# Kernel tuning notes

Measured on AMD Instinct MI355X. Metric: run time of the kernel, lower is better.

## Reference

```python
import jax, jax.numpy as jnp
import numpy as np

B, H, W, C = 2, 96, 96, 96
GROUPS = 32
EPS = 1e-5


def group_norm_dim1(x, gamma, beta):
    # Faithful to torch nn.GroupNorm(32, C) applied to an NHWC tensor:
    # dim 1 (H) is treated as the channel axis, normalized over (H//G, W, C) per group.
    b, h, w, c = x.shape
    xg = x.reshape(b, GROUPS, h // GROUPS, w, c)
    mean = xg.mean(axis=(2, 3, 4), keepdims=True)
    var = xg.var(axis=(2, 3, 4), keepdims=True)
    xn = ((xg - mean) * jax.lax.rsqrt(var + EPS)).reshape(b, h, w, c)
    return xn * gamma[None, :, None, None] + beta[None, :, None, None]


def setup_inputs() -> dict:
    key = jax.random.key(0)
    ks = jax.random.split(key, 9)
    s = 1.0 / np.sqrt(C)  # kaiming-uniform-ish scale
    x = jax.random.normal(ks[0], (B, H, W, C), dtype=jnp.float32)
    Wq = jax.random.uniform(ks[1], (C, C), jnp.float32, -s, s)
    Wk = jax.random.uniform(ks[2], (C, C), jnp.float32, -s, s)
    Wv = jax.random.uniform(ks[3], (C, C), jnp.float32, -s, s)
    Wp = jax.random.uniform(ks[4], (C, C), jnp.float32, -s, s)
    return {
        "x": x,
        "gamma": jnp.ones((H,), jnp.float32),   # GroupNorm affine weight (over dim 1)
        "beta": jnp.zeros((H,), jnp.float32),
        "Wq": Wq, "bq": jnp.zeros((C,), jnp.float32),
        "Wk": Wk, "bk": jnp.zeros((C,), jnp.float32),
        "Wv": Wv, "bv": jnp.zeros((C,), jnp.float32),
        "Wp": Wp, "bp": jnp.zeros((C,), jnp.float32),
    }


def reference(x, gamma, beta, Wq, bq, Wk, bk, Wv, bv, Wp, bp):
    b, h, w, c = x.shape
    hn = group_norm_dim1(x, gamma, beta)
    q = hn @ Wq + bq  # [B,H,W,C], Nin = contract last dim
    k = hn @ Wk + bk
    v = hn @ Wv + bv
    scale = c ** (-0.5)
    # full dense spatial attention: [B, HW, HW]
    scores = jnp.einsum('bxyc,buvc->bxyuv', q, k) * scale
    attn = jax.nn.softmax(scores.reshape(b, h, w, h * w), axis=-1).reshape(b, h, w, h, w)
    o = jnp.einsum('bxyuv,buvc->bxyc', attn, v)
    return x + (o @ Wp + bp)
```

## Files before the change

### kernel.cpp

```cpp
#include <hip/hip_runtime.h>
#include <hip/hip_bf16.h>
#include <stdint.h>

#define B_   2
#define H_   96
#define W_   96
#define C_   96
#define HW_  (H_ * W_)
#define NT_  (B_ * HW_)
#define EPS_ 1e-5f
#define SCL (0.10206207261596575f * 1.4426950408889634f)

typedef __hip_bfloat16 bf16;
typedef __attribute__((ext_vector_type(8))) short short8;
typedef __attribute__((ext_vector_type(16))) float f32x16;

__device__ __forceinline__ uint32_t pk_bf16(float a, float b) {
    uint32_t ua = __float_as_uint(a) + 0x8000u;
    uint32_t ub = __float_as_uint(b) + 0x8000u;
    return __builtin_amdgcn_perm(ub, ua, 0x07060302u);
}
__device__ __forceinline__ float bl(uint32_t u) { uint32_t x = u << 16;         return *(float*)&x; }
__device__ __forceinline__ float bh(uint32_t u) { uint32_t x = u & 0xffff0000u; return *(float*)&x; }
__device__ __forceinline__ float fexp2(float x) { return __builtin_amdgcn_exp2f(x); }
__device__ __forceinline__ short8 lds_frag(const short* p) {
    union { int2 h[2]; short8 v; } t;
    t.h[0] = *(const int2*)(p);
    t.h[1] = *(const int2*)(p + 4);
    return t.v;
}

__device__ __forceinline__ void load_hn_frags(
        const float* __restrict__ x, const float2* __restrict__ stats,
        const float* __restrict__ gamma, const float* __restrict__ beta,
        int token, int hh, short8* hf) {
    int b = token / HW_;
    int h = (token % HW_) / W_;
    float2 st = stats[b * 32 + h / 3];
    float g0 = gamma[h];
    float ga = g0 * st.y;
    float be = beta[h] - st.x * st.y * g0;
    const float* xr = x + (size_t)token * C_ + hh * 8;
    #pragma unroll
    for (int s = 0; s < 6; ++s) {
        float4 a = *(const float4*)(xr + s * 16);
        float4 c = *(const float4*)(xr + s * 16 + 4);
        union { uint32_t w[4]; short8 v; } f;
        f.w[0] = pk_bf16(a.x * ga + be, a.y * ga + be);
        f.w[1] = pk_bf16(a.z * ga + be, a.w * ga + be);
        f.w[2] = pk_bf16(c.x * ga + be, c.y * ga + be);
        f.w[3] = pk_bf16(c.z * ga + be, c.w * ga + be);
        hf[s] = f.v;
    }
}

__global__ __launch_bounds__(1024)
void stats_prep_kernel(const float* __restrict__ x, float2* __restrict__ stats,
                       const float* __restrict__ Wq, const float* __restrict__ Wk,
                       const float* __restrict__ Wv, const float* __restrict__ Wp,
                       bf16* __restrict__ wqt, bf16* __restrict__ wkt,
                       bf16* __restrict__ wvt, bf16* __restrict__ wpt) {
    int blk = blockIdx.x;
    int tid = threadIdx.x;
    if (blk >= 64) {
        int wsel = blk - 64;
        const float* S = (wsel == 0) ? Wq : (wsel == 1) ? Wk : (wsel == 2) ? Wv : Wp;
        bf16* D = (wsel == 0) ? wqt : (wsel == 1) ? wkt : (wsel == 2) ? wvt : wpt;
        for (int i = tid; i < C_ * C_; i += 1024) {
            int r = i / C_, c = i % C_;
            D[c * C_ + r] = __float2bfloat16(S[r * C_ + c]);
        }
        return;
    }
    int b = blk >> 5, g = blk & 31;
    const int n4 = 3 * W_ * C_ / 4;
    const float4* xb = (const float4*)(x + (size_t)(b * H_ + 3 * g) * (W_ * C_));
    float s = 0.f, ss = 0.f;
    for (int i = tid; i < n4; i += 1024) {
        float4 v = xb[i];
        s  += v.x + v.y + v.z + v.w;
        ss += v.x * v.x + v.y * v.y + v.z * v.z + v.w * v.w;
    }
    #pragma unroll
    for (int off = 1; off < 64; off <<= 1) {
        s  += __shfl_xor(s, off, 64);
        ss += __shfl_xor(ss, off, 64);
    }
    __shared__ float rs[16], rss[16];
    int wid = tid >> 6;
    if ((tid & 63) == 0) { rs[wid] = s; rss[wid] = ss; }
    __syncthreads();
    if (tid == 0) {
        float ts = 0.f, tss = 0.f;
        #pragma unroll
        for (int i = 0; i < 16; ++i) { ts += rs[i]; tss += rss[i]; }
        const float n = 3 * W_ * C_;
        float mean = ts / n;
        float var  = tss / n - mean * mean;
        stats[blk] = make_float2(mean, rsqrtf(var + EPS_));
    }
}

__global__ __launch_bounds__(64)
void qkv_kernel(const float* __restrict__ x, const float2* __restrict__ stats,
                const float* __restrict__ gamma, const float* __restrict__ beta,
                const bf16* __restrict__ wqt, const bf16* __restrict__ wkt,
                const bf16* __restrict__ wvt,
                const float* __restrict__ bq, const float* __restrict__ bk,
                const float* __restrict__ bv,
                bf16* __restrict__ qb, bf16* __restrict__ kb, bf16* __restrict__ vt) {
    __shared__ short tile_s[96 * 36];

    int blk = blockIdx.x;
    int w = blk / 576, tile = blk % 576;
    int n0 = tile * 32;
    int lane = threadIdx.x;
    int col = lane & 31, hh = lane >> 5;
    int token = n0 + col;

    short8 hf[6];
    load_hn_frags(x, stats, gamma, beta, token, hh, hf);

    if (w == 2) {
        int bb = n0 / HW_, nl0 = n0 % HW_;
        #pragma unroll
        for (int t = 0; t < 3; ++t) {
            int c = t * 32 + col;
            const bf16* wrow = wvt + (size_t)c * C_ + hh * 8;
            f32x16 acc = (f32x16)(0.f);
            #pragma unroll
            for (int s = 0; s < 6; ++s)
                acc = __builtin_amdgcn_mfma_f32_32x32x16_bf16(
                        hf[s], *(const short8*)(wrow + s * 16), acc, 0, 0, 0);
            float bias = bv[c];
            short* dst = tile_s + c * 36 + 4 * hh;
            #pragma unroll
            for (int g = 0; g < 4; ++g) {
                int2 pk = make_int2(pk_bf16(acc[4 * g] + bias, acc[4 * g + 1] + bias),
                                    pk_bf16(acc[4 * g + 2] + bias, acc[4 * g + 3] + bias));
                *(int2*)(dst + 8 * g) = pk;
            }
        }
        __syncthreads();
        bf16* vbase = vt + (size_t)bb * C_ * HW_ + nl0;
        #pragma unroll
        for (int i = 0; i < 6; ++i) {
            int pos = lane + 64 * i;
            int ch = pos >> 2, q4 = pos & 3;
            short8 vv = lds_frag(tile_s + ch * 36 + q4 * 8);
            *(short8*)(vbase + (size_t)ch * HW_ + q4 * 8) = vv;
        }
    } else {
        const bf16*  wt   = (w == 0) ? wqt : wkt;
        const float* bias = (w == 0) ? bq : bk;
        bf16*        dst  = (w == 0) ? qb : kb;
        float        scl  = (w == 0) ? SCL : 1.f;
        #pragma unroll
        for (int t = 0; t < 3; ++t) {
            const bf16* wrow = wt + (size_t)(t * 32 + col) * C_ + hh * 8;
            f32x16 acc = (f32x16)(0.f);
            #pragma unroll
            for (int s = 0; s < 6; ++s)
                acc = __builtin_amdgcn_mfma_f32_32x32x16_bf16(
                        *(const short8*)(wrow + s * 16), hf[s], acc, 0, 0, 0);
            #pragma unroll
            for (int g = 0; g < 4; ++g) {
                int nb = t * 32 + 8 * g + 4 * hh;
                float4 b4 = *(const float4*)(bias + nb);
                float v0 = (acc[4 * g]     + b4.x) * scl;
                float v1 = (acc[4 * g + 1] + b4.y) * scl;
                float v2 = (acc[4 * g + 2] + b4.z) * scl;
                float v3 = (acc[4 * g + 3] + b4.w) * scl;
                *(int2*)(tile_s + col * 100 + nb) =
                    make_int2(pk_bf16(v0, v1), pk_bf16(v2, v3));
            }
        }
        __syncthreads();
        bf16* dbase = dst + (size_t)n0 * C_;
        #pragma unroll
        for (int i = 0; i < 6; ++i) {
            int pos = lane + 64 * i;
            int tok = pos / 12, ch8 = (pos % 12) * 8;
            short8 vv = lds_frag(tile_s + tok * 100 + ch8);
            *(short8*)(dbase + tok * C_ + ch8) = vv;
        }
    }
}

template<int KS, int LOG2KS>
__global__ __launch_bounds__(256, 2)
void attn_kernel(const bf16* __restrict__ qb, const bf16* __restrict__ kb,
                 const bf16* __restrict__ vt,
                 bf16* __restrict__ pob, float* __restrict__ pl) {
    constexpr int KRANGE  = HW_ / KS;
    constexpr int ATT_NIT = KRANGE / 32;

    __shared__ short Kbuf[2][32 * 100];
    __shared__ short Vbuf[2][96 * 36];

    int blk = blockIdx.x;
    int ks = blk & (KS - 1), qg = blk >> LOG2KS;
    int b = qg / 36, g36 = qg % 36;
    int n0 = g36 * 256;
    int tid = threadIdx.x;
    int wave = tid >> 6, lane = tid & 63;
    int col = lane & 31, hh = lane >> 5;

    const bf16* kbb = kb + ((size_t)b * HW_ + (size_t)ks * KRANGE) * C_;
    const bf16* vbb = vt + (size_t)b * C_ * HW_ + (size_t)ks * KRANGE;

    int nA = n0 + wave * 32 + col;
    int nB = nA + 128;
    short8 qfA[6], qfB[6];
    {
        const bf16* qrowA = qb + (size_t)(b * HW_ + nA) * C_ + hh * 8;
        const bf16* qrowB = qb + (size_t)(b * HW_ + nB) * C_ + hh * 8;
        #pragma unroll
        for (int s = 0; s < 6; ++s) qfA[s] = *(const short8*)(qrowA + s * 16);
        #pragma unroll
        for (int s = 0; s < 6; ++s) qfB[s] = *(const short8*)(qrowB + s * 16);
    }

    f32x16 oaA[3], oaB[3];
    #pragma unroll
    for (int t = 0; t < 3; ++t) { oaA[t] = (f32x16)(0.f); oaB[t] = (f32x16)(0.f); }
    float lA = 0.f, lB = 0.f;

    bool isK = (tid < 128);
    int t128 = tid & 127;
    int ldsA[3], ldsB[3], goff[3];
    #pragma unroll
    for (int j = 0; j < 3; ++j) {
        int c = t128 + 128 * j;
        if (isK) {
            ldsA[j] = (c / 12) * 100 + (c % 12) * 8;
            ldsB[j] = ldsA[j] + 4;
            goff[j] = c * 8;
        } else {
            int rw = c >> 2, g = c & 3;
            ldsA[j] = rw * 36 + (2 * g - (g & 1)) * 4;
            ldsB[j] = rw * 36 + (2 * g + 2 - (g & 1)) * 4;
            goff[j] = rw * HW_ + g * 8;
        }
    }
    const bf16* gbase = isK ? kbb : vbb;
    const int itstep = isK ? (32 * C_) : 32;

    {
        short* sb = isK ? Kbuf[0] : Vbuf[0];
        #pragma unroll
        for (int j = 0; j < 3; ++j) {
            int4 r = *(const int4*)(gbase + goff[j]);
            *(int2*)(sb + ldsA[j]) = make_int2(r.x, r.y);
            *(int2*)(sb + ldsB[j]) = make_int2(r.z, r.w);
        }
    }
    __syncthreads();

    union FU { uint32_t w[4]; short8 v; };

    for (int it = 0; it < ATT_NIT; ++it) {
        int cur = it & 1;
        bool pre = (it + 1 < ATT_NIT);
        int4 r0, r1, r2;
        if (pre) {
            const bf16* g = gbase + (size_t)(it + 1) * itstep;
            r0 = *(const int4*)(g + goff[0]);
            r1 = *(const int4*)(g + goff[1]);
            r2 = *(const int4*)(g + goff[2]);
        }

        const short* Kc = Kbuf[cur];
        const short* Vc = Vbuf[cur];

        short8 kf[6];
        #pragma unroll
        for (int s = 0; s < 6; ++s)
            kf[s] = lds_frag(Kc + col * 100 + s * 16 + hh * 8);

        f32x16 stA = (f32x16)(0.f);
        #pragma unroll
        for (int s = 0; s < 6; ++s)
            stA = __builtin_amdgcn_mfma_f32_32x32x16_bf16(kf[s], qfA[s], stA, 0, 0, 0);
        f32x16 stB = (f32x16)(0.f);
        #pragma unroll
        for (int s = 0; s < 6; ++s)
            stB = __builtin_amdgcn_mfma_f32_32x32x16_bf16(kf[s], qfB[s], stB, 0, 0, 0);

        FU f0A, f1A, f0B, f1B;
        {
            float p[16], ls = 0.f;
            #pragma unroll
            for (int i = 0; i < 16; ++i) { p[i] = fexp2(stA[i]); ls += p[i]; }
            lA += ls;
            #pragma unroll
            for (int j = 0; j < 4; ++j) {
                f0A.w[j] = pk_bf16(p[2 * j],     p[2 * j + 1]);
                f1A.w[j] = pk_bf16(p[8 + 2 * j], p[8 + 2 * j + 1]);
            }
        }
        {
            float p[16], ls = 0.f;
            #pragma unroll
            for (int i = 0; i < 16; ++i) { p[i] = fexp2(stB[i]); ls += p[i]; }
            lB += ls;
            #pragma unroll
            for (int j = 0; j < 4; ++j) {
                f0B.w[j] = pk_bf16(p[2 * j],     p[2 * j + 1]);
                f1B.w[j] = pk_bf16(p[8 + 2 * j], p[8 + 2 * j + 1]);
            }
        }

        #pragma unroll
        for (int t = 0; t < 3; ++t) {
            const short* vr = Vc + (32 * t + col) * 36 + hh * 8;
            short8 vf0 = lds_frag(vr);
            short8 vf1 = lds_frag(vr + 16);
            oaA[t] = __builtin_amdgcn_mfma_f32_32x32x16_bf16(vf0, f0A.v, oaA[t], 0, 0, 0);
            oaA[t] = __builtin_amdgcn_mfma_f32_32x32x16_bf16(vf1, f1A.v, oaA[t], 0, 0, 0);
            oaB[t] = __builtin_amdgcn_mfma_f32_32x32x16_bf16(vf0, f0B.v, oaB[t], 0, 0, 0);
            oaB[t] = __builtin_amdgcn_mfma_f32_32x32x16_bf16(vf1, f1B.v, oaB[t], 0, 0, 0);
        }

        if (pre) {
            short* sb = isK ? Kbuf[cur ^ 1] : Vbuf[cur ^ 1];
            *(int2*)(sb + ldsA[0]) = make_int2(r0.x, r0.y);
            *(int2*)(sb + ldsB[0]) = make_int2(r0.z, r0.w);
            *(int2*)(sb + ldsA[1]) = make_int2(r1.x, r1.y);
            *(int2*)(sb + ldsB[1]) = make_int2(r1.z, r1.w);
            *(int2*)(sb + ldsA[2]) = make_int2(r2.x, r2.y);
            *(int2*)(sb + ldsB[2]) = make_int2(r2.z, r2.w);
        }
        __syncthreads();
    }

    {
        size_t bqA = (size_t)b * HW_ + nA;
        size_t bqB = (size_t)b * HW_ + nB;
        float ltA = lA + __shfl_xor(lA, 32, 64);
        float ltB = lB + __shfl_xor(lB, 32, 64);
        if (hh == 0) {
            pl[(size_t)ks * NT_ + bqA] = ltA;
            pl[(size_t)ks * NT_ + bqB] = ltB;
        }
        #pragma unroll
        for (int t = 0; t < 3; ++t)
            #pragma unroll
            for (int g = 0; g < 4; ++g) {
                int c0 = t * 32 + 8 * g + 4 * hh;
                uint2 pkA = make_uint2(
                    pk_bf16(oaA[t][4 * g],     oaA[t][4 * g + 1]),
                    pk_bf16(oaA[t][4 * g + 2], oaA[t][4 * g + 3]));
                *(uint2*)(pob + ((size_t)ks * NT_ + bqA) * C_ + c0) = pkA;
                uint2 pkB = make_uint2(
                    pk_bf16(oaB[t][4 * g],     oaB[t][4 * g + 1]),
                    pk_bf16(oaB[t][4 * g + 2], oaB[t][4 * g + 3]));
                *(uint2*)(pob + ((size_t)ks * NT_ + bqB) * C_ + c0) = pkB;
            }
    }
}

template<int KS>
__global__ __launch_bounds__(256)
void out_kernel(const float* __restrict__ x,
                const bf16* __restrict__ pob, const float* __restrict__ pl,
                const bf16* __restrict__ wpt, const float* __restrict__ bp,
                float* __restrict__ out) {
    __shared__ short ofs[32 * 100];
    __shared__ float linv_s[32];

    int tile = blockIdx.x;
    int n0 = tile * 32;
    int tid = threadIdx.x;

    if (tid < 32) {
        int token = n0 + tid;
        float l = 0.f;
        #pragma unroll
        for (int ksp = 0; ksp < KS; ++ksp) l += pl[(size_t)ksp * NT_ + token];
        linv_s[tid] = 1.f / l;
    }
    __syncthreads();

    for (int pos = tid; pos < 384; pos += 256) {
        int token = pos / 12, c8 = (pos % 12) * 8;
        float acc[8] = {0.f, 0.f, 0.f, 0.f, 0.f, 0.f, 0.f, 0.f};
        #pragma unroll
        for (int ksp = 0; ksp < KS; ++ksp) {
            uint4 u = *(const uint4*)(pob + ((size_t)ksp * NT_ + n0 + token) * C_ + c8);
            acc[0] += bl(u.x); acc[1] += bh(u.x);
            acc[2] += bl(u.y); acc[3] += bh(u.y);
            acc[4] += bl(u.z); acc[5] += bh(u.z);
            acc[6] += bl(u.w); acc[7] += bh(u.w);
        }
        float inv = linv_s[token];
        short* dst = ofs + token * 100 + c8;
        *(int2*)(dst)     = make_int2(pk_bf16(acc[0] * inv, acc[1] * inv),
                                      pk_bf16(acc[2] * inv, acc[3] * inv));
        *(int2*)(dst + 4) = make_int2(pk_bf16(acc[4] * inv, acc[5] * inv),
                                      pk_bf16(acc[6] * inv, acc[7] * inv));
    }
    __syncthreads();

    int wave = tid >> 6;
    if (wave >= 3) return;
    int lane = tid & 63, col = lane & 31, hh = lane >> 5;
    int t = wave;
    int token = n0 + col;

    short8 of[6];
    #pragma unroll
    for (int s = 0; s < 6; ++s)
        of[s] = lds_frag(ofs + col * 100 + s * 16 + hh * 8);

    f32x16 acc = (f32x16)(0.f);
    const bf16* wrow = wpt + (size_t)(t * 32 + col) * C_ + hh * 8;
    #pragma unroll
    for (int s = 0; s < 6; ++s)
        acc = __builtin_amdgcn_mfma_f32_32x32x16_bf16(
                *(const short8*)(wrow + s * 16), of[s], acc, 0, 0, 0);
    #pragma unroll
    for (int g = 0; g < 4; ++g) {
        int nb = t * 32 + 8 * g + 4 * hh;
        float4 b4 = *(const float4*)(bp + nb);
        float4 xv = *(const float4*)(x + (size_t)token * C_ + nb);
        float4 rr;
        rr.x = xv.x + acc[4 * g]     + b4.x;
        rr.y = xv.y + acc[4 * g + 1] + b4.y;
        rr.z = xv.z + acc[4 * g + 2] + b4.z;
        rr.w = xv.w + acc[4 * g + 3] + b4.w;
        *(float4*)(out + (size_t)token * C_ + nb) = rr;
    }
}

extern "C" void kernel_launch(void* const* d_in, const int* in_sizes, int n_in,
                              void* d_out, int out_size, void* d_ws, size_t ws_size,
                              hipStream_t stream) {
    const float* x     = (const float*)d_in[0];
    const float* gamma = (const float*)d_in[1];
    const float* beta  = (const float*)d_in[2];
    const float* Wq    = (const float*)d_in[3];
    const float* bq    = (const float*)d_in[4];
    const float* Wk    = (const float*)d_in[5];
    const float* bk    = (const float*)d_in[6];
    const float* Wv    = (const float*)d_in[7];
    const float* bv    = (const float*)d_in[8];
    const float* Wp    = (const float*)d_in[9];
    const float* bp    = (const float*)d_in[10];
    float* out = (float*)d_out;

    char* ws = (char*)d_ws;
    const size_t TB = (size_t)NT_ * C_ * 2;
    bf16* qb  = (bf16*)(ws);
    bf16* kb  = (bf16*)(ws + TB);
    bf16* vt  = (bf16*)(ws + 2 * TB);
    bf16* wqt = (bf16*)(ws + 3 * TB);
    bf16* wkt = (bf16*)(ws + 3 * TB + 18432);
    bf16* wvt = (bf16*)(ws + 3 * TB + 2 * 18432);
    bf16* wpt = (bf16*)(ws + 3 * TB + 3 * 18432);
    float2* stats = (float2*)(ws + 3 * TB + 4 * 18432);
    bf16*  pob = (bf16*)(ws + 3 * TB + 4 * 18432 + 512);

    hipLaunchKernelGGL(stats_prep_kernel, dim3(68), dim3(1024), 0, stream,
                       x, stats, Wq, Wk, Wv, Wp, wqt, wkt, wvt, wpt);
    hipLaunchKernelGGL(qkv_kernel, dim3(3 * 576), dim3(64), 0, stream,
                       x, stats, gamma, beta, wqt, wkt, wvt, bq, bk, bv, qb, kb, vt);

    const size_t base   = 3 * TB + 4 * 18432 + 512;
    const size_t need16 = base + (size_t)16 * NT_ * C_ * 2 + (size_t)16 * NT_ * 4;
    if (ws_size >= need16) {
        float* pl = (float*)(ws + base + (size_t)16 * NT_ * C_ * 2);
        hipLaunchKernelGGL((attn_kernel<16, 4>), dim3(16 * 72), dim3(256), 0, stream,
                           qb, kb, vt, pob, pl);
        hipLaunchKernelGGL((out_kernel<16>), dim3(576), dim3(256), 0, stream,
                           x, pob, pl, wpt, bp, out);
    } else {
        float* pl = (float*)(ws + base + (size_t)8 * NT_ * C_ * 2);
        hipLaunchKernelGGL((attn_kernel<8, 3>), dim3(8 * 72), dim3(256), 0, stream,
                           qb, kb, vt, pob, pl);
        hipLaunchKernelGGL((out_kernel<8>), dim3(576), dim3(256), 0, stream,
                           x, pob, pl, wpt, bp, out);
    }
}
```

Baseline: 190.8 us.

## Shrink attention blocks to two waves with fixed 8-way key split and setprio

Replaces the templated 4-wave attention kernel (16- or 8-way key split chosen by workspace size) with a 2-wave, 128-query block kernel that always uses an 8-way key split over 1152 blocks. Each block's K/V staging is spread over fewer threads, which now issue six loads each. It also raises wave priority around the MFMA/exp section with s_setprio. The aim is better occupancy and scheduling, and less partial-output traffic and reduction work in out_kernel than the 16-split path. The cost is that each block re-stages the same K/V tiles for half as many queries.

```diff
diff --git a/kernel.cpp b/kernel.cpp
--- a/kernel.cpp
+++ b/kernel.cpp
@@ -9,6 +9,9 @@
 #define HW_  (H_ * W_)
 #define NT_  (B_ * HW_)
 #define EPS_ 1e-5f
+#define KSPLIT  8
+#define KRANGE  (HW_ / KSPLIT)
+#define ATT_NIT (KRANGE / 32)
 #define SCL (0.10206207261596575f * 1.4426950408889634f)
 
 typedef __hip_bfloat16 bf16;
@@ -187,21 +190,17 @@
     }
 }
 
-template<int KS, int LOG2KS>
-__global__ __launch_bounds__(256, 2)
+__global__ __launch_bounds__(128, 2)
 void attn_kernel(const bf16* __restrict__ qb, const bf16* __restrict__ kb,
                  const bf16* __restrict__ vt,
                  bf16* __restrict__ pob, float* __restrict__ pl) {
-    constexpr int KRANGE  = HW_ / KS;
-    constexpr int ATT_NIT = KRANGE / 32;
-
     __shared__ short Kbuf[2][32 * 100];
     __shared__ short Vbuf[2][96 * 36];
 
     int blk = blockIdx.x;
-    int ks = blk & (KS - 1), qg = blk >> LOG2KS;
-    int b = qg / 36, g36 = qg % 36;
-    int n0 = g36 * 256;
+    int ks = blk & 7, qg = blk >> 3;
+    int b = qg / 72, g72 = qg % 72;
+    int n0 = g72 * 128;
     int tid = threadIdx.x;
     int wave = tid >> 6, lane = tid & 63;
     int col = lane & 31, hh = lane >> 5;
@@ -210,7 +209,7 @@
     const bf16* vbb = vt + (size_t)b * C_ * HW_ + (size_t)ks * KRANGE;
 
     int nA = n0 + wave * 32 + col;
-    int nB = nA + 128;
+    int nB = nA + 64;
     short8 qfA[6], qfB[6];
     {
         const bf16* qrowA = qb + (size_t)(b * HW_ + nA) * C_ + hh * 8;
@@ -226,12 +225,12 @@
     for (int t = 0; t < 3; ++t) { oaA[t] = (f32x16)(0.f); oaB[t] = (f32x16)(0.f); }
     float lA = 0.f, lB = 0.f;
 
-    bool isK = (tid < 128);
-    int t128 = tid & 127;
-    int ldsA[3], ldsB[3], goff[3];
-    #pragma unroll
-    for (int j = 0; j < 3; ++j) {
-        int c = t128 + 128 * j;
+    bool isK = (tid < 64);
+    int t64 = tid & 63;
+    int ldsA[6], ldsB[6], goff[6];
+    #pragma unroll
+    for (int j = 0; j < 6; ++j) {
+        int c = t64 + 64 * j;
         if (isK) {
             ldsA[j] = (c / 12) * 100 + (c % 12) * 8;
             ldsB[j] = ldsA[j] + 4;
@@ -249,7 +248,7 @@
     {
         short* sb = isK ? Kbuf[0] : Vbuf[0];
         #pragma unroll
-        for (int j = 0; j < 3; ++j) {
+        for (int j = 0; j < 6; ++j) {
             int4 r = *(const int4*)(gbase + goff[j]);
             *(int2*)(sb + ldsA[j]) = make_int2(r.x, r.y);
             *(int2*)(sb + ldsB[j]) = make_int2(r.z, r.w);
@@ -262,12 +261,15 @@
     for (int it = 0; it < ATT_NIT; ++it) {
         int cur = it & 1;
         bool pre = (it + 1 < ATT_NIT);
-        int4 r0, r1, r2;
+        int4 r0, r1, r2, r3, r4, r5;
         if (pre) {
             const bf16* g = gbase + (size_t)(it + 1) * itstep;
             r0 = *(const int4*)(g + goff[0]);
             r1 = *(const int4*)(g + goff[1]);
             r2 = *(const int4*)(g + goff[2]);
+            r3 = *(const int4*)(g + goff[3]);
+            r4 = *(const int4*)(g + goff[4]);
+            r5 = *(const int4*)(g + goff[5]);
         }
 
         const short* Kc = Kbuf[cur];
@@ -278,6 +280,7 @@
         for (int s = 0; s < 6; ++s)
             kf[s] = lds_frag(Kc + col * 100 + s * 16 + hh * 8);
 
+        __builtin_amdgcn_s_setprio(1);
         f32x16 stA = (f32x16)(0.f);
         #pragma unroll
         for (int s = 0; s < 6; ++s)
@@ -321,6 +324,7 @@
             oaB[t] = __builtin_amdgcn_mfma_f32_32x32x16_bf16(vf0, f0B.v, oaB[t], 0, 0, 0);
             oaB[t] = __builtin_amdgcn_mfma_f32_32x32x16_bf16(vf1, f1B.v, oaB[t], 0, 0, 0);
         }
+        __builtin_amdgcn_s_setprio(0);
 
         if (pre) {
             short* sb = isK ? Kbuf[cur ^ 1] : Vbuf[cur ^ 1];
@@ -330,6 +334,12 @@
             *(int2*)(sb + ldsB[1]) = make_int2(r1.z, r1.w);
             *(int2*)(sb + ldsA[2]) = make_int2(r2.x, r2.y);
             *(int2*)(sb + ldsB[2]) = make_int2(r2.z, r2.w);
+            *(int2*)(sb + ldsA[3]) = make_int2(r3.x, r3.y);
+            *(int2*)(sb + ldsB[3]) = make_int2(r3.z, r3.w);
+            *(int2*)(sb + ldsA[4]) = make_int2(r4.x, r4.y);
+            *(int2*)(sb + ldsB[4]) = make_int2(r4.z, r4.w);
+            *(int2*)(sb + ldsA[5]) = make_int2(r5.x, r5.y);
+            *(int2*)(sb + ldsB[5]) = make_int2(r5.z, r5.w);
         }
         __syncthreads();
     }
@@ -360,7 +370,6 @@
     }
 }
 
-template<int KS>
 __global__ __launch_bounds__(256)
 void out_kernel(const float* __restrict__ x,
                 const bf16* __restrict__ pob, const float* __restrict__ pl,
@@ -377,7 +386,7 @@
         int token = n0 + tid;
         float l = 0.f;
         #pragma unroll
-        for (int ksp = 0; ksp < KS; ++ksp) l += pl[(size_t)ksp * NT_ + token];
+        for (int ksp = 0; ksp < KSPLIT; ++ksp) l += pl[(size_t)ksp * NT_ + token];
         linv_s[tid] = 1.f / l;
     }
     __syncthreads();
@@ -386,7 +395,7 @@
         int token = pos / 12, c8 = (pos % 12) * 8;
         float acc[8] = {0.f, 0.f, 0.f, 0.f, 0.f, 0.f, 0.f, 0.f};
         #pragma unroll
-        for (int ksp = 0; ksp < KS; ++ksp) {
+        for (int ksp = 0; ksp < KSPLIT; ++ksp) {
             uint4 u = *(const uint4*)(pob + ((size_t)ksp * NT_ + n0 + token) * C_ + c8);
             acc[0] += bl(u.x); acc[1] += bh(u.x);
             acc[2] += bl(u.y); acc[3] += bh(u.y);
@@ -460,25 +469,15 @@
     bf16* wpt = (bf16*)(ws + 3 * TB + 3 * 18432);
     float2* stats = (float2*)(ws + 3 * TB + 4 * 18432);
     bf16*  pob = (bf16*)(ws + 3 * TB + 4 * 18432 + 512);
+    float* pl  = (float*)(ws + 3 * TB + 4 * 18432 + 512
+                          + (size_t)KSPLIT * NT_ * C_ * 2);
 
     hipLaunchKernelGGL(stats_prep_kernel, dim3(68), dim3(1024), 0, stream,
                        x, stats, Wq, Wk, Wv, Wp, wqt, wkt, wvt, wpt);
     hipLaunchKernelGGL(qkv_kernel, dim3(3 * 576), dim3(64), 0, stream,
                        x, stats, gamma, beta, wqt, wkt, wvt, bq, bk, bv, qb, kb, vt);
-
-    const size_t base   = 3 * TB + 4 * 18432 + 512;
-    const size_t need16 = base + (size_t)16 * NT_ * C_ * 2 + (size_t)16 * NT_ * 4;
-    if (ws_size >= need16) {
-        float* pl = (float*)(ws + base + (size_t)16 * NT_ * C_ * 2);
-        hipLaunchKernelGGL((attn_kernel<16, 4>), dim3(16 * 72), dim3(256), 0, stream,
-                           qb, kb, vt, pob, pl);
-        hipLaunchKernelGGL((out_kernel<16>), dim3(576), dim3(256), 0, stream,
-                           x, pob, pl, wpt, bp, out);
-    } else {
-        float* pl = (float*)(ws + base + (size_t)8 * NT_ * C_ * 2);
-        hipLaunchKernelGGL((attn_kernel<8, 3>), dim3(8 * 72), dim3(256), 0, stream,
-                           qb, kb, vt, pob, pl);
-        hipLaunchKernelGGL((out_kernel<8>), dim3(576), dim3(256), 0, stream,
-                           x, pob, pl, wpt, bp, out);
-    }
-}
+    hipLaunchKernelGGL(attn_kernel, dim3(1152), dim3(128), 0, stream,
+                       qb, kb, vt, pob, pl);
+    hipLaunchKernelGGL(out_kernel, dim3(576), dim3(256), 0, stream,
+                       x, pob, pl, wpt, bp, out);
+}
```

Measured after the change: 219.5 us. 15.0% more time.
